# Kernel tuning notes

Hardware: AMD Instinct MI355X
Metric: run time of the kernel (lower is better)

The kernel has to match this reference:

```python
import jax, jax.numpy as jnp
import numpy as np

EPS_LN = 1e-5

def _ln(x, w, b):
    m = x.mean(-1, keepdims=True)
    v = x.var(-1, keepdims=True)  # biased var, matching torch LayerNorm
    return (x - m) / jnp.sqrt(v + EPS_LN) * w + b


def setup_inputs() -> dict:
    key = jax.random.key(0)
    ks = jax.random.split(key, 20)
    B, N, C = 8, 4096, 256
    def lin_w(k, i, o):
        return (jax.random.normal(k, (i, o), jnp.float32) / np.sqrt(i)).astype(jnp.float32)
    inp = {
        'xyz': jax.random.normal(ks[0], (B, N, 3), jnp.float32),
        'features': jax.random.normal(ks[1], (B, N, C), jnp.float32),
        # geo_mlp: Linear(10,32), LN(32), ReLU, Linear(32,16)
        'g_w1': lin_w(ks[2], 10, 32), 'g_b1': jnp.zeros((32,), jnp.float32),
        'g_lnw': jnp.ones((32,), jnp.float32), 'g_lnb': jnp.zeros((32,), jnp.float32),
        'g_w2': lin_w(ks[3], 32, 16), 'g_b2': jnp.zeros((16,), jnp.float32),
        # edge_pred: Linear(C+16,64), LN(64), ReLU, Linear(64,1), Sigmoid
        'e_w1': lin_w(ks[4], C + 16, 64), 'e_b1': jnp.zeros((64,), jnp.float32),
        'e_lnw': jnp.ones((64,), jnp.float32), 'e_lnb': jnp.zeros((64,), jnp.float32),
        'e_w2': lin_w(ks[5], 64, 1), 'e_b2': jnp.zeros((1,), jnp.float32),
        # edge_refine: Linear(C,C), LN(C), ReLU
        'r_w': lin_w(ks[6], C, C), 'r_b': jnp.zeros((C,), jnp.float32),
        'r_lnw': jnp.ones((C,), jnp.float32), 'r_lnb': jnp.zeros((C,), jnp.float32),
    }
    return inp


def reference(xyz, features, g_w1, g_b1, g_lnw, g_lnb, g_w2, g_b2,
              e_w1, e_b1, e_lnw, e_lnb, e_w2, e_b2, r_w, r_b, r_lnw, r_lnb):
    k = 16
    # KNN: pairwise negative squared distance, top-k largest = nearest
    sq = jnp.sum(xyz * xyz, axis=-1)                              # [B,N]
    pd = 2.0 * jnp.einsum('bnd,bmd->bnm', xyz, xyz) - sq[:, :, None] - sq[:, None, :]
    idx = jax.lax.top_k(pd, k)[1]                                 # [B,N,k]
    nbr = jax.vmap(lambda p, i: p[i])(xyz, idx)                   # [B,N,k,3]
    cen = nbr - nbr.mean(axis=2, keepdims=True)                   # centered neighborhoods
    cov = jnp.einsum('bnkc,bnkd->bncd', cen, cen) / k             # [B,N,3,3]
    trace = cov[..., 0, 0] + cov[..., 1, 1] + cov[..., 2, 2]
    det = jnp.clip(cov[..., 0, 0] * cov[..., 1, 1] * cov[..., 2, 2], 1e-8, None)
    std = jnp.std(cen, axis=2, ddof=1)                            # [B,N,3] (torch unbiased std)
    d = jnp.linalg.norm(cen, axis=3)                              # [B,N,k]
    mean_d = d.mean(axis=2)
    std_d = jnp.std(d, axis=2, ddof=1)
    t = trace + 1e-6
    geo = jnp.stack([trace, det, std[..., 0], std[..., 1], std[..., 2],
                     mean_d, std_d, std[..., 0] / t, std[..., 1] / t, std[..., 2] / t], axis=-1)
    geo = jax.nn.relu(_ln(geo @ g_w1 + g_b1, g_lnw, g_lnb)) @ g_w2 + g_b2    # [B,N,16]
    comb = jnp.concatenate([features, geo], axis=-1)
    edge_prob = jax.nn.sigmoid(jax.nn.relu(_ln(comb @ e_w1 + e_b1, e_lnw, e_lnb)) @ e_w2 + e_b2)
    refined = jax.nn.relu(_ln(features @ r_w + r_b, r_lnw, r_lnb))
    refined = features + refined * edge_prob
    return refined, edge_prob
```

## Files before the change

kernel.cpp:

```cpp
#include <hip/hip_runtime.h>
#include <math.h>

#define BATCH 8
#define NPTS  4096
#define CF    256
#define TOPK  16
#define TOTQ  (BATCH*NPTS)
#define EPOFF ((size_t)TOTQ*CF)

typedef __attribute__((ext_vector_type(8))) short bf16x8;
typedef __attribute__((ext_vector_type(4))) float f32x4;

__device__ __forceinline__ unsigned short f2bf(float x) {
    union { float f; unsigned u; } a; a.f = x;
    unsigned r = a.u + 0x7fffu + ((a.u >> 16) & 1u);
    return (unsigned short)(r >> 16);
}
__device__ __forceinline__ float bf2f(unsigned short h) {
    union { float f; unsigned u; } a; a.u = ((unsigned)h) << 16; return a.f;
}
__device__ __forceinline__ void gl_lds16(const void* g, void* l) {
    __builtin_amdgcn_global_load_lds(
        (const __attribute__((address_space(1))) unsigned int*)g,
        (__attribute__((address_space(3))) unsigned int*)l, 16, 0, 0);
}

__global__ __launch_bounds__(256) void prep_xyz_k(const float* __restrict__ xyz,
                                                  float4* __restrict__ tab) {
    int i = blockIdx.x*256 + threadIdx.x;
    if (i < TOTQ) {
        float x = xyz[3*i], y = xyz[3*i+1], z = xyz[3*i+2];
        tab[i] = make_float4(x, y, z, x*x + y*y + z*z);
    }
}

__global__ __launch_bounds__(256) void prep_w_k(
    const float* __restrict__ rw, const float* __restrict__ ew1,
    unsigned short* __restrict__ rwh, unsigned short* __restrict__ rwl,
    unsigned short* __restrict__ ewh, unsigned short* __restrict__ ewl)
{
    int t = blockIdx.x*256 + threadIdx.x;
    if (t < 65536) {
        int k = t >> 8, n = t & 255;
        float x = rw[t];
        unsigned short h = f2bf(x);
        unsigned short l = f2bf(x - bf2f(h));
        int dst = (((k>>5)*16 + (n>>4)) << 9) + ((k>>3)&3)*128 + (n&15)*8 + (k&7);
        rwh[dst] = h; rwl[dst] = l;
    }
    if (t < 288*64) {
        int k = t >> 6, n = t & 63;
        float x = (k < 272) ? ew1[k*64 + n] : 0.f;
        unsigned short h = f2bf(x);
        unsigned short l = f2bf(x - bf2f(h));
        int dst = (((k>>5)*4 + (n>>4)) << 9) + ((k>>3)&3)*128 + (n&15)*8 + (k&7);
        ewh[dst] = h; ewl[dst] = l;
    }
}

__global__ __launch_bounds__(256, 2) void knn_geo_k(
    const float4* __restrict__ tab,
    const float* __restrict__ g_w1, const float* __restrict__ g_b1,
    const float* __restrict__ g_lnw, const float* __restrict__ g_lnb,
    const float* __restrict__ g_w2, const float* __restrict__ g_b2,
    float* __restrict__ geo_out)
{
    __shared__ float2 lst[TOPK][256];
    __shared__ float4 coords[64][TOPK+1];
    __shared__ float s_w1[320], s_b1[32], s_lnw[32], s_lnb[32], s_w2[512], s_b2[16];

    const int tid = threadIdx.x;
    for (int v = tid; v < 320; v += 256) s_w1[v] = g_w1[v];
    for (int v = tid; v < 512; v += 256) s_w2[v] = g_w2[v];
    if (tid < 32) { s_b1[tid] = g_b1[tid]; s_lnw[tid] = g_lnw[tid]; s_lnb[tid] = g_lnb[tid]; }
    if (tid < 16) s_b2[tid] = g_b2[tid];

    const int ql = tid & 63;
    const int qg = blockIdx.x*64 + ql;
    const int b  = blockIdx.x >> 6;
    const float4* __restrict__ ctab = tab + b*NPTS;
    const int ibase = __builtin_amdgcn_readfirstlane((tid >> 6) << 10);

    float4 q4 = tab[qg];
    const float qx = q4.x, qy = q4.y, qz = q4.z, qs = q4.w;

    float vals[TOPK]; int idxs[TOPK];
    #pragma unroll
    for (int j = 0; j < TOPK; ++j) { vals[j] = -INFINITY; idxs[j] = 0; }
    int   cnt = 0;
    float thr = -INFINITY;

    auto flushbuf = [&]() {
        for (int e = 0; e < cnt; ++e) {
            float2 en = lst[e][tid];
            float pv = en.x;
            int   pj = __float_as_int(en.y);
            if (pv > vals[TOPK-1]) {
                #pragma unroll
                for (int j = TOPK-1; j >= 1; --j) {
                    bool shift = pv > vals[j-1];
                    bool place = (!shift) && (pv > vals[j]);
                    vals[j] = shift ? vals[j-1] : (place ? pv : vals[j]);
                    idxs[j] = shift ? idxs[j-1] : (place ? pj : idxs[j]);
                }
                if (pv > vals[0]) { vals[0] = pv; idxs[0] = pj; }
            }
        }
    };

    float4 cbuf[8];
    #pragma unroll
    for (int u = 0; u < 8; ++u) cbuf[u] = ctab[ibase + u];

    for (int ib = 0; ib < 1024; ib += 8) {
        float4 cur[8];
        #pragma unroll
        for (int u = 0; u < 8; ++u) cur[u] = cbuf[u];
        if (ib + 8 < 1024) {
            #pragma unroll
            for (int u = 0; u < 8; ++u) cbuf[u] = ctab[ibase + ib + 8 + u];
        }
        #pragma unroll
        for (int u = 0; u < 8; ++u) {
            float dot = fmaf(qx, cur[u].x, fmaf(qy, cur[u].y, qz*cur[u].z));
            float pd  = fmaf(2.f, dot, -(qs + cur[u].w));
            if (pd > thr) {
                lst[cnt][tid] = make_float2(pd, __int_as_float(ibase + ib + u));
                ++cnt;
            }
        }
        if (__any(cnt > 8)) { flushbuf(); cnt = 0; thr = vals[TOPK-1]; }
    }
    flushbuf();

    #pragma unroll
    for (int e = 0; e < TOPK; ++e)
        lst[e][tid] = make_float2(vals[e], __int_as_float(idxs[e]));
    __syncthreads();

    if (tid < 64) {
        const int q = tid;
        int p0 = 0, p1 = 0, p2 = 0, p3 = 0;
        float sx = 0, sy = 0, sz = 0;
        for (int r = 0; r < TOPK; ++r) {
            float2 h0 = lst[p0][q];
            float2 h1 = lst[p1][64 + q];
            float2 h2 = lst[p2][128 + q];
            float2 h3 = lst[p3][192 + q];
            float best = h0.x; int bj = __float_as_int(h0.y); int bs = 0;
            if (h1.x > best) { best = h1.x; bj = __float_as_int(h1.y); bs = 1; }
            if (h2.x > best) { best = h2.x; bj = __float_as_int(h2.y); bs = 2; }
            if (h3.x > best) { best = h3.x; bj = __float_as_int(h3.y); bs = 3; }
            p0 += (bs == 0); p1 += (bs == 1); p2 += (bs == 2); p3 += (bs == 3);
            float4 nb = ctab[bj];
            coords[q][r] = nb;
            sx += nb.x; sy += nb.y; sz += nb.z;
        }
        const float mx = sx/16.f, my = sy/16.f, mz = sz/16.f;
        float sxx = 0, syy = 0, szz = 0, sd = 0;
        float dist[TOPK];
        #pragma unroll
        for (int r = 0; r < TOPK; ++r) {
            float4 nb = coords[q][r];
            float cx = nb.x - mx, cy = nb.y - my, cz = nb.z - mz;
            sxx += cx*cx; syy += cy*cy; szz += cz*cz;
            float dd = sqrtf(cx*cx + cy*cy + cz*cz);
            dist[r] = dd; sd += dd;
        }
        const float md = sd/16.f;
        float sdd = 0;
        #pragma unroll
        for (int r = 0; r < TOPK; ++r) { float t = dist[r] - md; sdd += t*t; }
        const float c00 = sxx/16.f, c11 = syy/16.f, c22 = szz/16.f;
        const float trace = c00 + c11 + c22;
        const float det = fmaxf(c00*c11*c22, 1e-8f);
        const float s0 = sqrtf(sxx/15.f), s1 = sqrtf(syy/15.f), s2 = sqrtf(szz/15.f);
        const float stdd = sqrtf(sdd/15.f);
        const float tt = trace + 1e-6f;
        float geo[10] = {trace, det, s0, s1, s2, md, stdd, s0/tt, s1/tt, s2/tt};

        float z1[32];
        #pragma unroll
        for (int jj = 0; jj < 32; ++jj) {
            float a = s_b1[jj];
            #pragma unroll
            for (int i = 0; i < 10; ++i) a = fmaf(geo[i], s_w1[i*32 + jj], a);
            z1[jj] = a;
        }
        float mzn = 0;
        #pragma unroll
        for (int jj = 0; jj < 32; ++jj) mzn += z1[jj];
        mzn /= 32.f;
        float vz = 0;
        #pragma unroll
        for (int jj = 0; jj < 32; ++jj) { float t = z1[jj] - mzn; vz += t*t; }
        vz /= 32.f;
        const float rs = 1.f/sqrtf(vz + 1e-5f);
        float h[32];
        #pragma unroll
        for (int jj = 0; jj < 32; ++jj)
            h[jj] = fmaxf((z1[jj]-mzn)*rs*s_lnw[jj] + s_lnb[jj], 0.f);
        float og[16];
        #pragma unroll
        for (int c = 0; c < 16; ++c) {
            float a = s_b2[c];
            #pragma unroll
            for (int i = 0; i < 32; ++i) a = fmaf(h[i], s_w2[i*16 + c], a);
            og[c] = a;
        }
        float4* gout = (float4*)(geo_out + (size_t)qg*16);
        gout[0] = make_float4(og[0],  og[1],  og[2],  og[3]);
        gout[1] = make_float4(og[4],  og[5],  og[6],  og[7]);
        gout[2] = make_float4(og[8],  og[9],  og[10], og[11]);
        gout[3] = make_float4(og[12], og[13], og[14], og[15]);
    }
}

__global__ __launch_bounds__(256, 1) void edge_k(
    const float* __restrict__ feat, const float* __restrict__ geo16,
    const unsigned short* __restrict__ rwh, const unsigned short* __restrict__ rwl,
    const unsigned short* __restrict__ ewh, const unsigned short* __restrict__ ewl,
    const float* __restrict__ e_b1, const float* __restrict__ e_lnw,
    const float* __restrict__ e_lnb, const float* __restrict__ e_w2,
    const float* __restrict__ e_b2,
    const float* __restrict__ r_b, const float* __restrict__ r_lnw,
    const float* __restrict__ r_lnb,
    float* __restrict__ out)
{
    __shared__ unsigned short sAh[64*296];
    __shared__ unsigned short sAl[64*296];
    __shared__ unsigned char  sB[65536];
    __shared__ float s_eb1[64], s_elnw[64], s_elnb[64], s_ew2[64];
    __shared__ float s_rb[256], s_rlnw[256], s_rlnb[256];
    __shared__ float s_ep[64], s_m[64], s_rs[64];
    __shared__ float sPx[256], sPq[256];

    const int tid  = threadIdx.x;
    const int lane = tid & 63;
    const int wv   = tid >> 6;
    const int lr   = lane & 15;
    const int lg   = lane >> 4;
    const int pbase = blockIdx.x * 64;

    if (tid < 64) { s_eb1[tid]=e_b1[tid]; s_elnw[tid]=e_lnw[tid]; s_elnb[tid]=e_lnb[tid]; s_ew2[tid]=e_w2[tid]; }
    s_rb[tid]=r_b[tid]; s_rlnw[tid]=r_lnw[tid]; s_rlnb[tid]=r_lnb[tid];

    const float4* f4 = (const float4*)(feat + (size_t)pbase*CF);
    #pragma unroll
    for (int it = 0; it < 16; ++it) {
        int v = tid + it*256;
        float4 x = f4[v];
        int row = v >> 6, c0 = (v & 63)*4;
        unsigned short h0=f2bf(x.x), h1=f2bf(x.y), h2=f2bf(x.z), h3=f2bf(x.w);
        unsigned short l0=f2bf(x.x-bf2f(h0)), l1=f2bf(x.y-bf2f(h1));
        unsigned short l2=f2bf(x.z-bf2f(h2)), l3=f2bf(x.w-bf2f(h3));
        *(ushort4*)&sAh[row*296 + c0] = make_ushort4(h0,h1,h2,h3);
        *(ushort4*)&sAl[row*296 + c0] = make_ushort4(l0,l1,l2,l3);
    }
    {
        const float4* g4 = (const float4*)(geo16 + (size_t)pbase*16);
        float4 x = g4[tid];
        int row = tid >> 2, c0 = 256 + (tid & 3)*4;
        unsigned short h0=f2bf(x.x), h1=f2bf(x.y), h2=f2bf(x.z), h3=f2bf(x.w);
        unsigned short l0=f2bf(x.x-bf2f(h0)), l1=f2bf(x.y-bf2f(h1));
        unsigned short l2=f2bf(x.z-bf2f(h2)), l3=f2bf(x.w-bf2f(h3));
        *(ushort4*)&sAh[row*296 + c0] = make_ushort4(h0,h1,h2,h3);
        *(ushort4*)&sAl[row*296 + c0] = make_ushort4(l0,l1,l2,l3);
        int zc = 272 + (tid & 3)*4;
        *(ushort4*)&sAh[row*296 + zc] = make_ushort4(0,0,0,0);
        *(ushort4*)&sAl[row*296 + zc] = make_ushort4(0,0,0,0);
    }

    auto stage3 = [&](int c, int buf) {
        const char* sh = (const char*)rwh + c*16384;
        const char* sl = (const char*)rwl + c*16384;
        char* dh = (char*)sB + buf*32768;
        char* dl = dh + 16384;
        #pragma unroll
        for (int i = 0; i < 4; ++i) {
            gl_lds16(sh + i*4096 + wv*1024 + lane*16, dh + i*4096 + wv*1024);
            gl_lds16(sl + i*4096 + wv*1024 + lane*16, dl + i*4096 + wv*1024);
        }
    };
    auto stage2 = [&](int c, int buf) {
        const char* sh = (const char*)ewh + c*4096;
        const char* sl = (const char*)ewl + c*4096;
        char* d = (char*)sB + 32768 + buf*8192;
        gl_lds16(sh + wv*1024 + lane*16, d + wv*1024);
        gl_lds16(sl + wv*1024 + lane*16, d + 4096 + wv*1024);
    };

    stage2(0, 0);
    stage3(0, 0);
    __syncthreads();

    f32x4 acc2[4];
    #pragma unroll
    for (int i = 0; i < 4; ++i) acc2[i] = (f32x4){0.f,0.f,0.f,0.f};
    const int arow2 = (wv*16 + lr)*296;
    for (int c = 0; c < 9; ++c) {
        if (c < 8) stage2(c+1, (c+1)&1);
        bf16x8 ah = *(const bf16x8*)&sAh[arow2 + c*32 + lg*8];
        bf16x8 al = *(const bf16x8*)&sAl[arow2 + c*32 + lg*8];
        const unsigned short* bb = (const unsigned short*)(sB + 32768 + (c&1)*8192);
        #pragma unroll
        for (int nt = 0; nt < 4; ++nt) {
            bf16x8 bh = *(const bf16x8*)&bb[nt*512 + lane*8];
            bf16x8 bl = *(const bf16x8*)&bb[2048 + nt*512 + lane*8];
            acc2[nt] = __builtin_amdgcn_mfma_f32_16x16x32_bf16(al, bh, acc2[nt], 0,0,0);
            acc2[nt] = __builtin_amdgcn_mfma_f32_16x16x32_bf16(ah, bl, acc2[nt], 0,0,0);
            acc2[nt] = __builtin_amdgcn_mfma_f32_16x16x32_bf16(ah, bh, acc2[nt], 0,0,0);
        }
        __syncthreads();
    }

    {
        float px[4] = {0,0,0,0}, pq[4] = {0,0,0,0};
        #pragma unroll
        for (int nt = 0; nt < 4; ++nt) {
            float bv = s_eb1[nt*16 + lr];
            #pragma unroll
            for (int j = 0; j < 4; ++j) {
                acc2[nt][j] += bv;
                px[j] += acc2[nt][j];
                pq[j] += acc2[nt][j]*acc2[nt][j];
            }
        }
        #pragma unroll
        for (int sw = 1; sw < 16; sw <<= 1) {
            #pragma unroll
            for (int j = 0; j < 4; ++j) { px[j] += __shfl_xor(px[j], sw); pq[j] += __shfl_xor(pq[j], sw); }
        }
        float mj[4], rj[4], dd[4] = {0,0,0,0};
        #pragma unroll
        for (int j = 0; j < 4; ++j) {
            mj[j] = px[j]*(1.f/64.f);
            float var = pq[j]*(1.f/64.f) - mj[j]*mj[j];
            rj[j] = rsqrtf(var + 1e-5f);
        }
        #pragma unroll
        for (int nt = 0; nt < 4; ++nt) {
            int col = nt*16 + lr;
            float lw = s_elnw[col], lb = s_elnb[col], w2 = s_ew2[col];
            #pragma unroll
            for (int j = 0; j < 4; ++j) {
                float h = fmaxf((acc2[nt][j]-mj[j])*rj[j]*lw + lb, 0.f);
                dd[j] = fmaf(h, w2, dd[j]);
            }
        }
        #pragma unroll
        for (int sw = 1; sw < 16; sw <<= 1) {
            #pragma unroll
            for (int j = 0; j < 4; ++j) dd[j] += __shfl_xor(dd[j], sw);
        }
        float eb2v = e_b2[0];
        #pragma unroll
        for (int j = 0; j < 4; ++j) {
            if (lr == j) {
                int row = wv*16 + lg*4 + j;
                float ep = 1.f/(1.f + expf(-(dd[j] + eb2v)));
                s_ep[row] = ep;
                out[EPOFF + pbase + row] = ep;
            }
        }
    }

    f32x4 acc3[4][4];
    #pragma unroll
    for (int mt = 0; mt < 4; ++mt)
        #pragma unroll
        for (int nt = 0; nt < 4; ++nt) acc3[mt][nt] = (f32x4){0.f,0.f,0.f,0.f};

    for (int c = 0; c < 8; ++c) {
        if (c < 7) stage3(c+1, (c+1)&1);
        bf16x8 ah[4], al[4];
        #pragma unroll
        for (int mt = 0; mt < 4; ++mt) {
            ah[mt] = *(const bf16x8*)&sAh[(mt*16+lr)*296 + c*32 + lg*8];
            al[mt] = *(const bf16x8*)&sAl[(mt*16+lr)*296 + c*32 + lg*8];
        }
        const unsigned short* bb = (const unsigned short*)(sB + (c&1)*32768);
        #pragma unroll
        for (int ntl = 0; ntl < 4; ++ntl) {
            int nt = wv*4 + ntl;
            bf16x8 bh = *(const bf16x8*)&bb[nt*512 + lane*8];
            bf16x8 bl = *(const bf16x8*)&bb[8192 + nt*512 + lane*8];
            #pragma unroll
            for (int mt = 0; mt < 4; ++mt) {
                acc3[mt][ntl] = __builtin_amdgcn_mfma_f32_16x16x32_bf16(al[mt], bh, acc3[mt][ntl], 0,0,0);
                acc3[mt][ntl] = __builtin_amdgcn_mfma_f32_16x16x32_bf16(ah[mt], bl, acc3[mt][ntl], 0,0,0);
                acc3[mt][ntl] = __builtin_amdgcn_mfma_f32_16x16x32_bf16(ah[mt], bh, acc3[mt][ntl], 0,0,0);
            }
        }
        __syncthreads();
    }

    float qx[4][4], qq[4][4];
    #pragma unroll
    for (int mt = 0; mt < 4; ++mt)
        #pragma unroll
        for (int j = 0; j < 4; ++j) { qx[mt][j] = 0.f; qq[mt][j] = 0.f; }
    #pragma unroll
    for (int ntl = 0; ntl < 4; ++ntl) {
        int col = (wv*4 + ntl)*16 + lr;
        float bv = s_rb[col];
        #pragma unroll
        for (int mt = 0; mt < 4; ++mt)
            #pragma unroll
            for (int j = 0; j < 4; ++j) {
                acc3[mt][ntl][j] += bv;
                float v = acc3[mt][ntl][j];
                qx[mt][j] += v; qq[mt][j] += v*v;
            }
    }
    #pragma unroll
    for (int sw = 1; sw < 16; sw <<= 1) {
        #pragma unroll
        for (int mt = 0; mt < 4; ++mt)
            #pragma unroll
            for (int j = 0; j < 4; ++j) { qx[mt][j] += __shfl_xor(qx[mt][j], sw); qq[mt][j] += __shfl_xor(qq[mt][j], sw); }
    }
    if (lr == 0) {
        #pragma unroll
        for (int mt = 0; mt < 4; ++mt)
            #pragma unroll
            for (int j = 0; j < 4; ++j) {
                int row = mt*16 + lg*4 + j;
                sPx[wv*64 + row] = qx[mt][j];
                sPq[wv*64 + row] = qq[mt][j];
            }
    }
    __syncthreads();
    if (tid < 64) {
        float Sx = sPx[tid] + sPx[64+tid] + sPx[128+tid] + sPx[192+tid];
        float Sq = sPq[tid] + sPq[64+tid] + sPq[128+tid] + sPq[192+tid];
        float m  = Sx*(1.f/256.f);
        float var = Sq*(1.f/256.f) - m*m;
        s_m[tid]  = m;
        s_rs[tid] = rsqrtf(var + 1e-5f);
    }
    __syncthreads();

    {
        float* sOut = (float*)sB;
        float lwv[4], lbv[4]; int colv[4];
        #pragma unroll
        for (int ntl = 0; ntl < 4; ++ntl) {
            colv[ntl] = (wv*4 + ntl)*16 + lr;
            lwv[ntl] = s_rlnw[colv[ntl]];
            lbv[ntl] = s_rlnb[colv[ntl]];
        }
        #pragma unroll
        for (int mt = 0; mt < 4; ++mt) {
            #pragma unroll
            for (int j = 0; j < 4; ++j) {
                int row = mt*16 + lg*4 + j;
                float m = s_m[row], rs = s_rs[row];
                #pragma unroll
                for (int ntl = 0; ntl < 4; ++ntl) {
                    float h = fmaxf((acc3[mt][ntl][j]-m)*rs*lwv[ntl] + lbv[ntl], 0.f);
                    sOut[row*256 + colv[ntl]] = h;
                }
            }
        }
    }
    __syncthreads();

    {
        const float* sOut = (const float*)sB;
        #pragma unroll
        for (int it = 0; it < 16; ++it) {
            int v = tid + it*256;
            int row = v >> 6, c0 = (v & 63)*4;
            float4 h4 = *(const float4*)&sOut[row*256 + c0];
            ushort4 hh = *(const ushort4*)&sAh[row*296 + c0];
            ushort4 ll = *(const ushort4*)&sAl[row*296 + c0];
            float ep = s_ep[row];
            float4 o;
            o.x = bf2f(hh.x) + bf2f(ll.x) + h4.x*ep;
            o.y = bf2f(hh.y) + bf2f(ll.y) + h4.y*ep;
            o.z = bf2f(hh.z) + bf2f(ll.z) + h4.z*ep;
            o.w = bf2f(hh.w) + bf2f(ll.w) + h4.w*ep;
            *(float4*)&out[(size_t)(pbase+row)*CF + c0] = o;
        }
    }
}

extern "C" void kernel_launch(void* const* d_in, const int* in_sizes, int n_in,
                              void* d_out, int out_size, void* d_ws, size_t ws_size,
                              hipStream_t stream) {
    (void)in_sizes; (void)n_in; (void)out_size; (void)ws_size;
    const float* xyz   = (const float*)d_in[0];
    const float* feat  = (const float*)d_in[1];
    const float* g_w1  = (const float*)d_in[2];
    const float* g_b1  = (const float*)d_in[3];
    const float* g_lnw = (const float*)d_in[4];
    const float* g_lnb = (const float*)d_in[5];
    const float* g_w2  = (const float*)d_in[6];
    const float* g_b2  = (const float*)d_in[7];
    const float* e_w1  = (const float*)d_in[8];
    const float* e_b1  = (const float*)d_in[9];
    const float* e_lnw = (const float*)d_in[10];
    const float* e_lnb = (const float*)d_in[11];
    const float* e_w2  = (const float*)d_in[12];
    const float* e_b2  = (const float*)d_in[13];
    const float* r_w   = (const float*)d_in[14];
    const float* r_b   = (const float*)d_in[15];
    const float* r_lnw = (const float*)d_in[16];
    const float* r_lnb = (const float*)d_in[17];
    float* out = (float*)d_out;

    char* ws = (char*)d_ws;
    float*          geo_ws = (float*)ws;
    float4*         tab    = (float4*)(ws + 0x200000);
    unsigned short* rwh    = (unsigned short*)(ws + 0x280000);
    unsigned short* rwl    = (unsigned short*)(ws + 0x2A0000);
    unsigned short* ewh    = (unsigned short*)(ws + 0x2C0000);
    unsigned short* ewl    = (unsigned short*)(ws + 0x2D0000);

    hipLaunchKernelGGL(prep_xyz_k, dim3(TOTQ/256), dim3(256), 0, stream, xyz, tab);
    hipLaunchKernelGGL(prep_w_k, dim3(256), dim3(256), 0, stream,
                       r_w, e_w1, rwh, rwl, ewh, ewl);
    hipLaunchKernelGGL(knn_geo_k, dim3(TOTQ/64), dim3(256), 0, stream,
                       tab, g_w1, g_b1, g_lnw, g_lnb, g_w2, g_b2, geo_ws);
    hipLaunchKernelGGL(edge_k, dim3(TOTQ/64), dim3(256), 0, stream,
                       feat, geo_ws, rwh, rwl, ewh, ewl,
                       e_b1, e_lnw, e_lnb, e_w2, e_b2,
                       r_b, r_lnw, r_lnb, out);
}
```

Baseline: 282.4 us.

## Split KNN scan across eight waves with two-stage top-k merge and fused prep

Each query's candidate scan now runs across 8 wavefronts of 512 points each, up from 4 waves of 1024, so blocks grow to 512 threads with a two-stage merge of per-wave top-16 lists through shared memory. The insertion step now uses branch-free fmin/fmax selects, the flush threshold is tighter, and the two prep kernels are merged into one launch. This aims to raise parallelism and latency hiding in the dominant KNN kernel. In exchange it adds extra barriers and a serial merge pass on a single wave, and register pressure goes up under the new launch bounds.

```diff
diff --git a/kernel.cpp b/kernel.cpp
--- a/kernel.cpp
+++ b/kernel.cpp
@@ -25,21 +25,17 @@
         (__attribute__((address_space(3))) unsigned int*)l, 16, 0, 0);
 }
 
-__global__ __launch_bounds__(256) void prep_xyz_k(const float* __restrict__ xyz,
-                                                  float4* __restrict__ tab) {
-    int i = blockIdx.x*256 + threadIdx.x;
-    if (i < TOTQ) {
-        float x = xyz[3*i], y = xyz[3*i+1], z = xyz[3*i+2];
-        tab[i] = make_float4(x, y, z, x*x + y*y + z*z);
-    }
-}
-
-__global__ __launch_bounds__(256) void prep_w_k(
+__global__ __launch_bounds__(256) void prep_k(
+    const float* __restrict__ xyz, float4* __restrict__ tab,
     const float* __restrict__ rw, const float* __restrict__ ew1,
     unsigned short* __restrict__ rwh, unsigned short* __restrict__ rwl,
     unsigned short* __restrict__ ewh, unsigned short* __restrict__ ewl)
 {
     int t = blockIdx.x*256 + threadIdx.x;
+    if (t < TOTQ) {
+        float x = xyz[3*t], y = xyz[3*t+1], z = xyz[3*t+2];
+        tab[t] = make_float4(x, y, z, x*x + y*y + z*z);
+    }
     if (t < 65536) {
         int k = t >> 8, n = t & 255;
         float x = rw[t];
@@ -58,28 +54,30 @@
     }
 }
 
-__global__ __launch_bounds__(256, 2) void knn_geo_k(
+__global__ __launch_bounds__(512, 4) void knn_geo_k(
     const float4* __restrict__ tab,
     const float* __restrict__ g_w1, const float* __restrict__ g_b1,
     const float* __restrict__ g_lnw, const float* __restrict__ g_lnb,
     const float* __restrict__ g_w2, const float* __restrict__ g_b2,
     float* __restrict__ geo_out)
 {
-    __shared__ float2 lst[TOPK][256];
+    __shared__ float2 lstS[8][512];
+    __shared__ float2 M1[16][64];
     __shared__ float4 coords[64][TOPK+1];
     __shared__ float s_w1[320], s_b1[32], s_lnw[32], s_lnb[32], s_w2[512], s_b2[16];
 
     const int tid = threadIdx.x;
-    for (int v = tid; v < 320; v += 256) s_w1[v] = g_w1[v];
-    for (int v = tid; v < 512; v += 256) s_w2[v] = g_w2[v];
+    if (tid < 320) s_w1[tid] = g_w1[tid];
+    s_w2[tid & 511] = g_w2[tid & 511];
     if (tid < 32) { s_b1[tid] = g_b1[tid]; s_lnw[tid] = g_lnw[tid]; s_lnb[tid] = g_lnb[tid]; }
     if (tid < 16) s_b2[tid] = g_b2[tid];
 
     const int ql = tid & 63;
     const int qg = blockIdx.x*64 + ql;
+    const int wv = tid >> 6;
     const int b  = blockIdx.x >> 6;
     const float4* __restrict__ ctab = tab + b*NPTS;
-    const int ibase = __builtin_amdgcn_readfirstlane((tid >> 6) << 10);
+    const int ibase = __builtin_amdgcn_readfirstlane(wv << 9);
 
     float4 q4 = tab[qg];
     const float qx = q4.x, qy = q4.y, qz = q4.z, qs = q4.w;
@@ -92,66 +90,102 @@
 
     auto flushbuf = [&]() {
         for (int e = 0; e < cnt; ++e) {
-            float2 en = lst[e][tid];
+            float2 en = lstS[e][tid];
             float pv = en.x;
             int   pj = __float_as_int(en.y);
             if (pv > vals[TOPK-1]) {
                 #pragma unroll
                 for (int j = TOPK-1; j >= 1; --j) {
-                    bool shift = pv > vals[j-1];
-                    bool place = (!shift) && (pv > vals[j]);
-                    vals[j] = shift ? vals[j-1] : (place ? pv : vals[j]);
-                    idxs[j] = shift ? idxs[j-1] : (place ? pj : idxs[j]);
+                    bool ca = pv > vals[j];
+                    bool cb = pv > vals[j-1];
+                    float t = fminf(pv, vals[j-1]);
+                    vals[j] = fmaxf(vals[j], t);
+                    int ish = cb ? idxs[j-1] : pj;
+                    idxs[j] = ca ? ish : idxs[j];
                 }
-                if (pv > vals[0]) { vals[0] = pv; idxs[0] = pj; }
+                bool c0 = pv > vals[0];
+                idxs[0] = c0 ? pj : idxs[0];
+                vals[0] = fmaxf(vals[0], pv);
             }
         }
     };
 
-    float4 cbuf[8];
-    #pragma unroll
-    for (int u = 0; u < 8; ++u) cbuf[u] = ctab[ibase + u];
-
-    for (int ib = 0; ib < 1024; ib += 8) {
-        float4 cur[8];
-        #pragma unroll
-        for (int u = 0; u < 8; ++u) cur[u] = cbuf[u];
-        if (ib + 8 < 1024) {
-            #pragma unroll
-            for (int u = 0; u < 8; ++u) cbuf[u] = ctab[ibase + ib + 8 + u];
-        }
-        #pragma unroll
-        for (int u = 0; u < 8; ++u) {
-            float dot = fmaf(qx, cur[u].x, fmaf(qy, cur[u].y, qz*cur[u].z));
-            float pd  = fmaf(2.f, dot, -(qs + cur[u].w));
-            if (pd > thr) {
-                lst[cnt][tid] = make_float2(pd, __int_as_float(ibase + ib + u));
-                ++cnt;
-            }
-        }
-        if (__any(cnt > 8)) { flushbuf(); cnt = 0; thr = vals[TOPK-1]; }
-    }
-    flushbuf();
-
-    #pragma unroll
-    for (int e = 0; e < TOPK; ++e)
-        lst[e][tid] = make_float2(vals[e], __int_as_float(idxs[e]));
-    __syncthreads();
-
+    #define EVALC(c, gi)                                                     \
+        {                                                                    \
+            float dot = fmaf(qx, (c).x, fmaf(qy, (c).y, qz*(c).z));          \
+            float pd  = fmaf(2.f, dot, -(qs + (c).w));                       \
+            if (pd > thr) {                                                  \
+                lstS[cnt][tid] = make_float2(pd, __int_as_float(gi));        \
+                ++cnt;                                                       \
+            }                                                                \
+        }
+
+    {
+        const float4* cptr = ctab + ibase;
+        float4 A0 = cptr[0], A1 = cptr[1], A2 = cptr[2], A3 = cptr[3];
+        for (int ib = 0; ib < 512; ib += 8) {
+            float4 B0 = cptr[ib+4], B1 = cptr[ib+5], B2 = cptr[ib+6], B3 = cptr[ib+7];
+            EVALC(A0, ibase+ib+0); EVALC(A1, ibase+ib+1);
+            EVALC(A2, ibase+ib+2); EVALC(A3, ibase+ib+3);
+            if (__any(cnt > 4)) { flushbuf(); cnt = 0; thr = vals[TOPK-1]; }
+            A0 = cptr[ib+8]; A1 = cptr[ib+9]; A2 = cptr[ib+10]; A3 = cptr[ib+11];
+            EVALC(B0, ibase+ib+4); EVALC(B1, ibase+ib+5);
+            EVALC(B2, ibase+ib+6); EVALC(B3, ibase+ib+7);
+            if (__any(cnt > 4)) { flushbuf(); cnt = 0; thr = vals[TOPK-1]; }
+        }
+        flushbuf();
+    }
+    #undef EVALC
+
+    float2 (*lstP)[256] = (float2(*)[256])&lstS[0][0];
+
+    __syncthreads();
+    if (wv < 4) {
+        #pragma unroll
+        for (int e = 0; e < TOPK; ++e)
+            lstP[e][wv*64 + ql] = make_float2(vals[e], __int_as_float(idxs[e]));
+    }
+    __syncthreads();
     if (tid < 64) {
         const int q = tid;
         int p0 = 0, p1 = 0, p2 = 0, p3 = 0;
-        float sx = 0, sy = 0, sz = 0;
         for (int r = 0; r < TOPK; ++r) {
-            float2 h0 = lst[p0][q];
-            float2 h1 = lst[p1][64 + q];
-            float2 h2 = lst[p2][128 + q];
-            float2 h3 = lst[p3][192 + q];
+            float2 h0 = lstP[p0][q];
+            float2 h1 = lstP[p1][64 + q];
+            float2 h2 = lstP[p2][128 + q];
+            float2 h3 = lstP[p3][192 + q];
             float best = h0.x; int bj = __float_as_int(h0.y); int bs = 0;
             if (h1.x > best) { best = h1.x; bj = __float_as_int(h1.y); bs = 1; }
             if (h2.x > best) { best = h2.x; bj = __float_as_int(h2.y); bs = 2; }
             if (h3.x > best) { best = h3.x; bj = __float_as_int(h3.y); bs = 3; }
             p0 += (bs == 0); p1 += (bs == 1); p2 += (bs == 2); p3 += (bs == 3);
+            M1[r][q] = make_float2(best, __int_as_float(bj));
+        }
+    }
+    __syncthreads();
+    if (wv >= 4) {
+        #pragma unroll
+        for (int e = 0; e < TOPK; ++e)
+            lstP[e][(wv-4)*64 + ql] = make_float2(vals[e], __int_as_float(idxs[e]));
+    }
+    __syncthreads();
+
+    if (tid < 64) {
+        const int q = tid;
+        int pm = 0, p4 = 0, p5 = 0, p6 = 0, p7 = 0;
+        float sx = 0, sy = 0, sz = 0;
+        for (int r = 0; r < TOPK; ++r) {
+            float2 hm = M1[pm][q];
+            float2 h4 = lstP[p4][q];
+            float2 h5 = lstP[p5][64 + q];
+            float2 h6 = lstP[p6][128 + q];
+            float2 h7 = lstP[p7][192 + q];
+            float best = hm.x; int bj = __float_as_int(hm.y); int bs = 0;
+            if (h4.x > best) { best = h4.x; bj = __float_as_int(h4.y); bs = 1; }
+            if (h5.x > best) { best = h5.x; bj = __float_as_int(h5.y); bs = 2; }
+            if (h6.x > best) { best = h6.x; bj = __float_as_int(h6.y); bs = 3; }
+            if (h7.x > best) { best = h7.x; bj = __float_as_int(h7.y); bs = 4; }
+            pm += (bs == 0); p4 += (bs == 1); p5 += (bs == 2); p6 += (bs == 3); p7 += (bs == 4);
             float4 nb = ctab[bj];
             coords[q][r] = nb;
             sx += nb.x; sy += nb.y; sz += nb.z;
@@ -196,16 +230,15 @@
         for (int jj = 0; jj < 32; ++jj) { float t = z1[jj] - mzn; vz += t*t; }
         vz /= 32.f;
         const float rs = 1.f/sqrtf(vz + 1e-5f);
-        float h[32];
         #pragma unroll
         for (int jj = 0; jj < 32; ++jj)
-            h[jj] = fmaxf((z1[jj]-mzn)*rs*s_lnw[jj] + s_lnb[jj], 0.f);
+            z1[jj] = fmaxf((z1[jj]-mzn)*rs*s_lnw[jj] + s_lnb[jj], 0.f);
         float og[16];
         #pragma unroll
         for (int c = 0; c < 16; ++c) {
             float a = s_b2[c];
             #pragma unroll
-            for (int i = 0; i < 32; ++i) a = fmaf(h[i], s_w2[i*16 + c], a);
+            for (int i = 0; i < 32; ++i) a = fmaf(z1[i], s_w2[i*16 + c], a);
             og[c] = a;
         }
         float4* gout = (float4*)(geo_out + (size_t)qg*16);
@@ -518,10 +551,9 @@
     unsigned short* ewh    = (unsigned short*)(ws + 0x2C0000);
     unsigned short* ewl    = (unsigned short*)(ws + 0x2D0000);
 
-    hipLaunchKernelGGL(prep_xyz_k, dim3(TOTQ/256), dim3(256), 0, stream, xyz, tab);
-    hipLaunchKernelGGL(prep_w_k, dim3(256), dim3(256), 0, stream,
-                       r_w, e_w1, rwh, rwl, ewh, ewl);
-    hipLaunchKernelGGL(knn_geo_k, dim3(TOTQ/64), dim3(256), 0, stream,
+    hipLaunchKernelGGL(prep_k, dim3(256), dim3(256), 0, stream,
+                       xyz, tab, r_w, e_w1, rwh, rwl, ewh, ewl);
+    hipLaunchKernelGGL(knn_geo_k, dim3(TOTQ/64), dim3(512), 0, stream,
                        tab, g_w1, g_b1, g_lnw, g_lnb, g_w2, g_b2, geo_ws);
     hipLaunchKernelGGL(edge_k, dim3(TOTQ/64), dim3(256), 0, stream,
                        feat, geo_ws, rwh, rwl, ewh, ewl,
```

Result: slower. 314.9 us (+11.5%).
